# Kernel tuning notes

Measured on AMD Instinct MI355X. Metric: run time of the kernel, lower is better.

The kernel has to match this reference:

```python
import jax, jax.numpy as jnp
import numpy as np

EPS = 1e-12  # keras K.l2_normalize epsilon


def _l2_normalize(v, axis):
    return v * jax.lax.rsqrt(jnp.maximum(jnp.sum(v * v, axis=axis, keepdims=True), EPS))


def setup_inputs() -> dict:
    key = jax.random.key(0)
    k1, k2, k3, k4 = jax.random.split(key, 4)
    B, T, D, K, O = 32, 1024, 512, 64, 1024
    x = jax.random.normal(k1, (B, T, D), dtype=jnp.float32)
    weight = jax.random.normal(k2, (D, K), dtype=jnp.float32) * (1.0 / np.sqrt(D))
    bias = jnp.zeros((K,), dtype=jnp.float32)
    centers = jax.random.normal(k3, (K, D), dtype=jnp.float32)
    reduc_dim = jax.random.normal(k4, (D * K, O), dtype=jnp.float32) * 0.01
    return {"x": x, "weight": weight, "bias": bias, "centers": centers, "reduc_dim": reduc_dim}


def reference(x, weight, bias, centers, reduc_dim):
    # x: [B,T,D], weight: [D,K], bias: [K]
    # soft assignment: softmax over centers
    a = jax.nn.softmax(jnp.einsum('btd,dk->btk', x, weight) + bias, axis=-1)  # [B,T,K]
    # aggregate descriptors per center: batch_dot over time axis -> [B,K,D]
    x_agg = jnp.einsum('btk,btd->bkd', a, x)
    # total soft weight per center: [B,K]
    sum_w = jnp.sum(a, axis=1)
    # residual vs centers, broadcast: [B,K,D]
    full = x_agg - sum_w[:, :, None] * centers[None, :, :]
    # intra-normalize per center vector
    full = _l2_normalize(full, axis=-1)
    B = x.shape[0]
    full = full.reshape(B, -1)  # [B, K*D]
    full = _l2_normalize(full, axis=-1)
    return full @ reduc_dim  # [B, output_dim]
```

## Files before the change

### kernel.cpp

```cpp
#include <hip/hip_runtime.h>
#include <math.h>

#define TT 1024
#define DD 512
#define KK 64
#define OO 1024
#define EPSF 1e-12f

typedef __attribute__((ext_vector_type(8))) short bf16x8;
typedef __attribute__((ext_vector_type(4))) float f32x4;

__device__ __forceinline__ ushort f2bf(float f) {
  unsigned u = __float_as_uint(f);
  u = (u + 0x7FFFu + ((u >> 16) & 1u)) >> 16;
  return (ushort)u;
}
__device__ __forceinline__ float bf2f(ushort h) {
  return __uint_as_float(((unsigned)h) << 16);
}


__global__ __launch_bounds__(256) void nv_k0(const float* __restrict__ w,
                                             ushort* __restrict__ whT,
                                             float* __restrict__ sum_w) {
  int idx = blockIdx.x * 256 + threadIdx.x;
  if (idx < 32768) {
    int d = idx >> 6, k = idx & 63;
    whT[(size_t)k * DD + d] = f2bf(w[idx]);
  } else if (idx < 32768 + 2048) {
    sum_w[idx - 32768] = 0.f;
  }
}

__global__ __launch_bounds__(256) void nv_k1(
    const float* __restrict__ x, const ushort* __restrict__ whT,
    const float* __restrict__ bias, ushort* __restrict__ aT,
    ushort* __restrict__ xbfT, float* __restrict__ sum_w) {
  const int b = blockIdx.y, t0 = blockIdx.x * 64;
  const int tid = threadIdx.x;
  const int wave = tid >> 6, lane = tid & 63, l15 = lane & 15, q = lane >> 4;

  __shared__ ushort xs[64 * 64];
  __shared__ ushort xsT[64 * 64];
  __shared__ ushort wsm[64 * 64];

  f32x4 acc[4];
#pragma unroll
  for (int nt = 0; nt < 4; ++nt)
#pragma unroll
    for (int r = 0; r < 4; ++r) acc[nt][r] = 0.f;

  for (int dc = 0; dc < DD; dc += 64) {
    __syncthreads();
#pragma unroll
    for (int it = 0; it < 2; ++it) {
      int gi = it * 256 + tid;
      int t = gi >> 3, gd = gi & 7;
      const float* px = x + (size_t)(b * TT + t0 + t) * DD + dc + gd * 8;
      float4 v0 = *(const float4*)px;
      float4 v1 = *(const float4*)(px + 4);
      ushort u[8];
      u[0] = f2bf(v0.x); u[1] = f2bf(v0.y); u[2] = f2bf(v0.z); u[3] = f2bf(v0.w);
      u[4] = f2bf(v1.x); u[5] = f2bf(v1.y); u[6] = f2bf(v1.z); u[7] = f2bf(v1.w);
      bf16x8 pk;
#pragma unroll
      for (int i = 0; i < 8; ++i) pk[i] = (short)u[i];
      *(bf16x8*)(xs + t * 64 + ((gd ^ (t & 7)) << 3)) = pk;
      int tg = t >> 3;
#pragma unroll
      for (int i = 0; i < 8; ++i) {
        int d = gd * 8 + i;
        xsT[d * 64 + ((tg ^ ((d >> 3) & 7)) << 3) + (t & 7)] = u[i];
      }
    }
#pragma unroll
    for (int it = 0; it < 2; ++it) {
      int gi = it * 256 + tid;
      int k = gi >> 3, gd = gi & 7;
      bf16x8 v = *(const bf16x8*)(whT + (size_t)k * DD + dc + gd * 8);
      *(bf16x8*)(wsm + k * 64 + ((gd ^ (k & 7)) << 3)) = v;
    }
    __syncthreads();
#pragma unroll
    for (int kc = 0; kc < 2; ++kc) {
      int gq = kc * 4 + q;
      int t = wave * 16 + l15;
      bf16x8 af = *(const bf16x8*)(xs + t * 64 + ((gq ^ (t & 7)) << 3));
#pragma unroll
      for (int nt = 0; nt < 4; ++nt) {
        int k = nt * 16 + l15;
        bf16x8 bfv = *(const bf16x8*)(wsm + k * 64 + ((gq ^ (k & 7)) << 3));
        acc[nt] = __builtin_amdgcn_mfma_f32_16x16x32_bf16(af, bfv, acc[nt], 0, 0, 0);
      }
    }
#pragma unroll
    for (int it = 0; it < 2; ++it) {
      int gi = it * 256 + tid;
      int d = gi >> 3, g = gi & 7;
      bf16x8 v = *(const bf16x8*)(xsT + d * 64 + (g << 3));
      int tg = g ^ ((d >> 3) & 7);
      *(bf16x8*)(xbfT + (size_t)(b * DD + dc + d) * TT + t0 + tg * 8) = v;
    }
  }

  float bia[4];
#pragma unroll
  for (int nt = 0; nt < 4; ++nt) bia[nt] = bias[nt * 16 + l15];

  ushort au[4][4];
  float sw[4] = {0.f, 0.f, 0.f, 0.f};
#pragma unroll
  for (int r = 0; r < 4; ++r) {
    float l[4];
#pragma unroll
    for (int nt = 0; nt < 4; ++nt) l[nt] = acc[nt][r] + bia[nt];
    float m = fmaxf(fmaxf(l[0], l[1]), fmaxf(l[2], l[3]));
#pragma unroll
    for (int s = 1; s <= 8; s <<= 1) m = fmaxf(m, __shfl_xor(m, s));
    float e[4];
#pragma unroll
    for (int nt = 0; nt < 4; ++nt) e[nt] = __expf(l[nt] - m);
    float ssum = e[0] + e[1] + e[2] + e[3];
#pragma unroll
    for (int s = 1; s <= 8; s <<= 1) ssum += __shfl_xor(ssum, s);
    float inv = 1.f / ssum;
#pragma unroll
    for (int nt = 0; nt < 4; ++nt) {
      ushort u = f2bf(e[nt] * inv);
      au[nt][r] = u;
      sw[nt] += bf2f(u);
    }
  }
#pragma unroll
  for (int nt = 0; nt < 4; ++nt) {
    float s = sw[nt];
    s += __shfl_xor(s, 16);
    s += __shfl_xor(s, 32);
    if (q == 0) atomicAdd(sum_w + b * KK + nt * 16 + l15, s);
  }
  __syncthreads();
#pragma unroll
  for (int nt = 0; nt < 4; ++nt)
#pragma unroll
    for (int r = 0; r < 4; ++r) {
      int k = nt * 16 + l15;
      int t = wave * 16 + q * 4 + r;
      xs[k * 64 + (((t >> 3) ^ (k & 7)) << 3) + (t & 7)] = au[nt][r];
    }
  __syncthreads();
#pragma unroll
  for (int it = 0; it < 2; ++it) {
    int gi = it * 256 + tid;
    int k = gi >> 3, g = gi & 7;
    bf16x8 v = *(const bf16x8*)(xs + k * 64 + (g << 3));
    int tg = g ^ (k & 7);
    *(bf16x8*)(aT + (size_t)(b * KK + k) * TT + t0 + tg * 8) = v;
  }
}

__global__ __launch_bounds__(256) void nv_k2(
    const ushort* __restrict__ aT, const ushort* __restrict__ xbfT,
    float* __restrict__ xaggP) {
  const int d0 = blockIdx.x * 64;
  const int b = blockIdx.y;
  const int tsp = blockIdx.z;
  const int tid = threadIdx.x;
  const int wave = tid >> 6, lane = tid & 63, l15 = lane & 15, q = lane >> 4;

  __shared__ ushort asx[64 * 64];
  __shared__ ushort xsb[64 * 64];

  f32x4 acc[4];
#pragma unroll
  for (int nt = 0; nt < 4; ++nt)
#pragma unroll
    for (int r = 0; r < 4; ++r) acc[nt][r] = 0.f;

  for (int tc = 0; tc < 4; ++tc) {
    const int t0 = tsp * 256 + tc * 64;
    __syncthreads();
#pragma unroll
    for (int it = 0; it < 2; ++it) {
      int gi = it * 256 + tid;
      int k = gi >> 3, g = gi & 7;
      bf16x8 v = *(const bf16x8*)(aT + (size_t)(b * KK + k) * TT + t0 + g * 8);
      *(bf16x8*)(asx + k * 64 + ((g ^ (k & 7)) << 3)) = v;
    }
#pragma unroll
    for (int it = 0; it < 2; ++it) {
      int gi = it * 256 + tid;
      int d = gi >> 3, g = gi & 7;
      bf16x8 v = *(const bf16x8*)(xbfT + (size_t)(b * DD + d0 + d) * TT + t0 + g * 8);
      *(bf16x8*)(xsb + d * 64 + ((g ^ (d & 7)) << 3)) = v;
    }
    __syncthreads();
#pragma unroll
    for (int kc = 0; kc < 2; ++kc) {
      int gq = kc * 4 + q;
      int k = wave * 16 + l15;
      bf16x8 af = *(const bf16x8*)(asx + k * 64 + ((gq ^ (k & 7)) << 3));
#pragma unroll
      for (int nt = 0; nt < 4; ++nt) {
        int d = nt * 16 + l15;
        bf16x8 bfv = *(const bf16x8*)(xsb + d * 64 + ((gq ^ (d & 7)) << 3));
        acc[nt] = __builtin_amdgcn_mfma_f32_16x16x32_bf16(af, bfv, acc[nt], 0, 0, 0);
      }
    }
  }
#pragma unroll
  for (int nt = 0; nt < 4; ++nt)
#pragma unroll
    for (int r = 0; r < 4; ++r) {
      int k = wave * 16 + q * 4 + r;
      xaggP[(size_t)((tsp * 32 + b) * KK + k) * DD + d0 + nt * 16 + l15] = acc[nt][r];
    }
}

__global__ __launch_bounds__(128) void nv_k3a(
    const float* __restrict__ xaggP, float* __restrict__ full,
    const float* __restrict__ centers, const float* __restrict__ sum_w,
    float* __restrict__ s1) {
  const int k = blockIdx.x, b = blockIdx.y;
  const int tid = threadIdx.x;
  const float sw = sum_w[b * KK + k];
  float4 v = make_float4(0.f, 0.f, 0.f, 0.f);
#pragma unroll
  for (int sp = 0; sp < 4; ++sp) {
    float4 p = *((const float4*)(xaggP + (size_t)((sp * 32 + b) * KK + k) * DD) + tid);
    v.x += p.x; v.y += p.y; v.z += p.z; v.w += p.w;
  }
  float4 c = *((const float4*)(centers + (size_t)k * DD) + tid);
  v.x = fmaf(-sw, c.x, v.x);
  v.y = fmaf(-sw, c.y, v.y);
  v.z = fmaf(-sw, c.z, v.z);
  v.w = fmaf(-sw, c.w, v.w);
  *((float4*)(full + (size_t)(b * KK + k) * DD) + tid) = v;
  float ss = v.x * v.x + v.y * v.y + v.z * v.z + v.w * v.w;
#pragma unroll
  for (int s = 1; s <= 32; s <<= 1) ss += __shfl_xor(ss, s);
  __shared__ float red[2];
  if ((tid & 63) == 0) red[tid >> 6] = ss;
  __syncthreads();
  if (tid == 0) s1[b * KK + k] = red[0] + red[1];
}

__global__ __launch_bounds__(64) void nv_k3b(const float* __restrict__ s1,
                                             float* __restrict__ scale) {
  const int b = blockIdx.x, k = threadIdx.x;
  float r = s1[b * KK + k];
  float d1 = fmaxf(r, EPSF);
  float s2 = r / d1;
#pragma unroll
  for (int s = 1; s <= 32; s <<= 1) s2 += __shfl_xor(s2, s);
  scale[b * KK + k] = rsqrtf(d1) * rsqrtf(fmaxf(s2, EPSF));
}

__global__ __launch_bounds__(128) void nv_k3c(const float* __restrict__ full,
                                              const float* __restrict__ scale,
                                              ushort* __restrict__ fullbf) {
  const int blk = blockIdx.x;
  const float sc = scale[blk];
  float4 v = *((const float4*)(full + (size_t)blk * DD) + threadIdx.x);
  ushort4 o;
  o.x = f2bf(v.x * sc); o.y = f2bf(v.y * sc);
  o.z = f2bf(v.z * sc); o.w = f2bf(v.w * sc);
  *((ushort4*)(fullbf + (size_t)blk * DD) + threadIdx.x) = o;
}

__global__ __launch_bounds__(256) void nv_k4(
    const ushort* __restrict__ fullbf, const float* __restrict__ reduc,
    float* __restrict__ outP) {
  const int c_base = blockIdx.x * 64;
  const int r_base = blockIdx.y * 512;
  const int tid = threadIdx.x;
  const int tx = tid & 15;
  const int ty = (tid >> 4) & 3;
  const int tz = tid >> 6;
  const int c0 = c_base + tx * 4;

  __shared__ float As2[32 * 128];

  float acc[8][4] = {};

  for (int ch = 0; ch < 4; ++ch) {
    const int rch = r_base + ch * 128;
    __syncthreads();
#pragma unroll
    for (int it = 0; it < 2; ++it) {
      int gi = it * 256 + tid;
      int bb = gi >> 4, g = gi & 15;
      bf16x8 v = *(const bf16x8*)(fullbf + (size_t)bb * 32768 + rch + g * 8);
      float4 lo, hi;
      lo.x = bf2f((ushort)v[0]); lo.y = bf2f((ushort)v[1]);
      lo.z = bf2f((ushort)v[2]); lo.w = bf2f((ushort)v[3]);
      hi.x = bf2f((ushort)v[4]); hi.y = bf2f((ushort)v[5]);
      hi.z = bf2f((ushort)v[6]); hi.w = bf2f((ushort)v[7]);
      *(float4*)(As2 + bb * 128 + g * 8) = lo;
      *(float4*)(As2 + bb * 128 + g * 8 + 4) = hi;
    }
    __syncthreads();
#pragma unroll 4
    for (int i = 0; i < 8; ++i) {
      const int rl = i * 16 + ty * 4;
      float wv[4][4];
#pragma unroll
      for (int j = 0; j < 4; ++j) {
        float4 w = *(const float4*)(reduc + (size_t)(rch + rl + j) * OO + c0);
        wv[j][0] = w.x; wv[j][1] = w.y; wv[j][2] = w.z; wv[j][3] = w.w;
      }
#pragma unroll
      for (int bb = 0; bb < 8; ++bb) {
        float4 a4 = *(const float4*)(As2 + (tz * 8 + bb) * 128 + rl);
        float a_[4] = {a4.x, a4.y, a4.z, a4.w};
#pragma unroll
        for (int j = 0; j < 4; ++j) {
          acc[bb][0] = fmaf(a_[j], wv[j][0], acc[bb][0]);
          acc[bb][1] = fmaf(a_[j], wv[j][1], acc[bb][1]);
          acc[bb][2] = fmaf(a_[j], wv[j][2], acc[bb][2]);
          acc[bb][3] = fmaf(a_[j], wv[j][3], acc[bb][3]);
        }
      }
    }
  }

#pragma unroll
  for (int bb = 0; bb < 8; ++bb) {
    float4 v = make_float4(acc[bb][0], acc[bb][1], acc[bb][2], acc[bb][3]);
    v.x += __shfl_xor(v.x, 16); v.x += __shfl_xor(v.x, 32);
    v.y += __shfl_xor(v.y, 16); v.y += __shfl_xor(v.y, 32);
    v.z += __shfl_xor(v.z, 16); v.z += __shfl_xor(v.z, 32);
    v.w += __shfl_xor(v.w, 16); v.w += __shfl_xor(v.w, 32);
    if (ty == 0) {
      *(float4*)(outP + (size_t)(blockIdx.y * 32 + tz * 8 + bb) * OO + c0) = v;
    }
  }
}

__global__ __launch_bounds__(256) void nv_k5(const float* __restrict__ outP,
                                             float* __restrict__ out) {
  const int idx = blockIdx.x * 256 + threadIdx.x;
  float s = 0.f;
#pragma unroll 8
  for (int sp = 0; sp < 64; ++sp) s += outP[(size_t)sp * 32768 + idx];
  out[idx] = s;
}

extern "C" void kernel_launch(void* const* d_in, const int* in_sizes, int n_in,
                              void* d_out, int out_size, void* d_ws, size_t ws_size,
                              hipStream_t stream) {
  const float* x = (const float*)d_in[0];
  const float* weight = (const float*)d_in[1];
  const float* bias = (const float*)d_in[2];
  const float* centers = (const float*)d_in[3];
  const float* reduc = (const float*)d_in[4];
  float* out = (float*)d_out;
  float* ws = (float*)d_ws;

  ushort* aT = (ushort*)ws;
  ushort* xbfT = (ushort*)(ws + 1048576);
  float* xaggP = ws + 9437184;
  float* full = ws + 13631488;
  ushort* fullbf = (ushort*)(ws + 14680064);
  float* outP = ws + 15728640;
  ushort* whT = (ushort*)(ws + 17825792);
  float* sum_w = ws + 17825792 + 16384;
  float* s1 = sum_w + 2048;
  float* scale = sum_w + 4096;

  nv_k0<<<136, 256, 0, stream>>>(weight, whT, sum_w);
  nv_k1<<<dim3(16, 32), 256, 0, stream>>>(x, whT, bias, aT, xbfT, sum_w);
  nv_k2<<<dim3(8, 32, 4), 256, 0, stream>>>(aT, xbfT, xaggP);
  nv_k3a<<<dim3(64, 32), 128, 0, stream>>>(xaggP, full, centers, sum_w, s1);
  nv_k3b<<<32, 64, 0, stream>>>(s1, scale);
  nv_k3c<<<2048, 128, 0, stream>>>(full, scale, fullbf);
  nv_k4<<<dim3(16, 64), 256, 0, stream>>>(fullbf, reduc, outP);
  nv_k5<<<128, 256, 0, stream>>>(outP, out);
}
```

Before: 319.4 us.

## Restructure final projection GEMM with transposed fp32 activations and wider split-K

```diff
diff --git a/kernel.cpp b/kernel.cpp
--- a/kernel.cpp
+++ b/kernel.cpp
@@ -257,82 +257,93 @@
 
 __global__ __launch_bounds__(128) void nv_k3c(const float* __restrict__ full,
                                               const float* __restrict__ scale,
-                                              ushort* __restrict__ fullbf) {
+                                              float* __restrict__ fullT) {
   const int blk = blockIdx.x;
+  const int b = blk >> 6, k = blk & 63;
   const float sc = scale[blk];
   float4 v = *((const float4*)(full + (size_t)blk * DD) + threadIdx.x);
-  ushort4 o;
-  o.x = f2bf(v.x * sc); o.y = f2bf(v.y * sc);
-  o.z = f2bf(v.z * sc); o.w = f2bf(v.w * sc);
-  *((ushort4*)(fullbf + (size_t)blk * DD) + threadIdx.x) = o;
-}
-
-__global__ __launch_bounds__(256) void nv_k4(
-    const ushort* __restrict__ fullbf, const float* __restrict__ reduc,
+  int r0 = k * DD + threadIdx.x * 4;
+  fullT[(size_t)(r0 + 0) * 32 + b] = v.x * sc;
+  fullT[(size_t)(r0 + 1) * 32 + b] = v.y * sc;
+  fullT[(size_t)(r0 + 2) * 32 + b] = v.z * sc;
+  fullT[(size_t)(r0 + 3) * 32 + b] = v.w * sc;
+}
+
+__global__ __launch_bounds__(256, 2) void nv_k4(
+    const float* __restrict__ fullT, const float* __restrict__ reduc,
     float* __restrict__ outP) {
-  const int c_base = blockIdx.x * 64;
-  const int r_base = blockIdx.y * 512;
+  const int strip = blockIdx.x;
+  const int ksp = blockIdx.y;
   const int tid = threadIdx.x;
-  const int tx = tid & 15;
-  const int ty = (tid >> 4) & 3;
-  const int tz = tid >> 6;
-  const int c0 = c_base + tx * 4;
-
-  __shared__ float As2[32 * 128];
-
-  float acc[8][4] = {};
-
-  for (int ch = 0; ch < 4; ++ch) {
-    const int rch = r_base + ch * 128;
-    __syncthreads();
-#pragma unroll
-    for (int it = 0; it < 2; ++it) {
-      int gi = it * 256 + tid;
-      int bb = gi >> 4, g = gi & 15;
-      bf16x8 v = *(const bf16x8*)(fullbf + (size_t)bb * 32768 + rch + g * 8);
-      float4 lo, hi;
-      lo.x = bf2f((ushort)v[0]); lo.y = bf2f((ushort)v[1]);
-      lo.z = bf2f((ushort)v[2]); lo.w = bf2f((ushort)v[3]);
-      hi.x = bf2f((ushort)v[4]); hi.y = bf2f((ushort)v[5]);
-      hi.z = bf2f((ushort)v[6]); hi.w = bf2f((ushort)v[7]);
-      *(float4*)(As2 + bb * 128 + g * 8) = lo;
-      *(float4*)(As2 + bb * 128 + g * 8 + 4) = hi;
-    }
-    __syncthreads();
-#pragma unroll 4
-    for (int i = 0; i < 8; ++i) {
-      const int rl = i * 16 + ty * 4;
-      float wv[4][4];
-#pragma unroll
-      for (int j = 0; j < 4; ++j) {
-        float4 w = *(const float4*)(reduc + (size_t)(rch + rl + j) * OO + c0);
-        wv[j][0] = w.x; wv[j][1] = w.y; wv[j][2] = w.z; wv[j][3] = w.w;
-      }
-#pragma unroll
-      for (int bb = 0; bb < 8; ++bb) {
-        float4 a4 = *(const float4*)(As2 + (tz * 8 + bb) * 128 + rl);
-        float a_[4] = {a4.x, a4.y, a4.z, a4.w};
-#pragma unroll
-        for (int j = 0; j < 4; ++j) {
-          acc[bb][0] = fmaf(a_[j], wv[j][0], acc[bb][0]);
-          acc[bb][1] = fmaf(a_[j], wv[j][1], acc[bb][1]);
-          acc[bb][2] = fmaf(a_[j], wv[j][2], acc[bb][2]);
-          acc[bb][3] = fmaf(a_[j], wv[j][3], acc[bb][3]);
+  const int wave = tid >> 6, lane = tid & 63;
+  const int c0 = strip * 256 + lane * 4;
+  const int kblk = ksp * 256;
+
+  __shared__ float fst[256 * 32];
+
+#pragma unroll
+  for (int it = 0; it < 8; ++it) {
+    int f4 = it * 256 + tid;
+    *(float4*)(fst + f4 * 4) = *(const float4*)(fullT + (size_t)kblk * 32 + f4 * 4);
+  }
+  __syncthreads();
+
+  float4 acc[32];
+#pragma unroll
+  for (int b = 0; b < 32; ++b) acc[b] = make_float4(0.f, 0.f, 0.f, 0.f);
+
+  const int kw = wave * 64;
+#pragma unroll 2
+  for (int kk = 0; kk < 64; ++kk) {
+    const int kl = kw + kk;
+    float4 rv = *(const float4*)(reduc + (size_t)(kblk + kl) * OO + c0);
+#pragma unroll
+    for (int b4 = 0; b4 < 8; ++b4) {
+      float4 fv = *(const float4*)(fst + kl * 32 + b4 * 4);
+      acc[b4 * 4 + 0].x = fmaf(fv.x, rv.x, acc[b4 * 4 + 0].x);
+      acc[b4 * 4 + 0].y = fmaf(fv.x, rv.y, acc[b4 * 4 + 0].y);
+      acc[b4 * 4 + 0].z = fmaf(fv.x, rv.z, acc[b4 * 4 + 0].z);
+      acc[b4 * 4 + 0].w = fmaf(fv.x, rv.w, acc[b4 * 4 + 0].w);
+      acc[b4 * 4 + 1].x = fmaf(fv.y, rv.x, acc[b4 * 4 + 1].x);
+      acc[b4 * 4 + 1].y = fmaf(fv.y, rv.y, acc[b4 * 4 + 1].y);
+      acc[b4 * 4 + 1].z = fmaf(fv.y, rv.z, acc[b4 * 4 + 1].z);
+      acc[b4 * 4 + 1].w = fmaf(fv.y, rv.w, acc[b4 * 4 + 1].w);
+      acc[b4 * 4 + 2].x = fmaf(fv.z, rv.x, acc[b4 * 4 + 2].x);
+      acc[b4 * 4 + 2].y = fmaf(fv.z, rv.y, acc[b4 * 4 + 2].y);
+      acc[b4 * 4 + 2].z = fmaf(fv.z, rv.z, acc[b4 * 4 + 2].z);
+      acc[b4 * 4 + 2].w = fmaf(fv.z, rv.w, acc[b4 * 4 + 2].w);
+      acc[b4 * 4 + 3].x = fmaf(fv.w, rv.x, acc[b4 * 4 + 3].x);
+      acc[b4 * 4 + 3].y = fmaf(fv.w, rv.y, acc[b4 * 4 + 3].y);
+      acc[b4 * 4 + 3].z = fmaf(fv.w, rv.z, acc[b4 * 4 + 3].z);
+      acc[b4 * 4 + 3].w = fmaf(fv.w, rv.w, acc[b4 * 4 + 3].w);
+    }
+  }
+
+  __syncthreads();
+  for (int w = 0; w < 4; ++w) {
+    if (wave == w) {
+      if (w == 0) {
+#pragma unroll
+        for (int b = 0; b < 32; ++b)
+          *(float4*)(fst + b * 256 + lane * 4) = acc[b];
+      } else {
+#pragma unroll
+        for (int b = 0; b < 32; ++b) {
+          float4 v = *(float4*)(fst + b * 256 + lane * 4);
+          v.x += acc[b].x; v.y += acc[b].y; v.z += acc[b].z; v.w += acc[b].w;
+          *(float4*)(fst + b * 256 + lane * 4) = v;
         }
       }
     }
-  }
-
-#pragma unroll
-  for (int bb = 0; bb < 8; ++bb) {
-    float4 v = make_float4(acc[bb][0], acc[bb][1], acc[bb][2], acc[bb][3]);
-    v.x += __shfl_xor(v.x, 16); v.x += __shfl_xor(v.x, 32);
-    v.y += __shfl_xor(v.y, 16); v.y += __shfl_xor(v.y, 32);
-    v.z += __shfl_xor(v.z, 16); v.z += __shfl_xor(v.z, 32);
-    v.w += __shfl_xor(v.w, 16); v.w += __shfl_xor(v.w, 32);
-    if (ty == 0) {
-      *(float4*)(outP + (size_t)(blockIdx.y * 32 + tz * 8 + bb) * OO + c0) = v;
-    }
+    __syncthreads();
+  }
+
+#pragma unroll
+  for (int it = 0; it < 8; ++it) {
+    int f4 = it * 256 + tid;
+    int b = f4 >> 6, cg = f4 & 63;
+    *(float4*)(outP + ((size_t)(ksp * 32 + b) * OO) + strip * 256 + cg * 4) =
+        *(const float4*)(fst + b * 256 + cg * 4);
   }
 }
 
@@ -341,7 +352,7 @@
   const int idx = blockIdx.x * 256 + threadIdx.x;
   float s = 0.f;
 #pragma unroll 8
-  for (int sp = 0; sp < 64; ++sp) s += outP[(size_t)sp * 32768 + idx];
+  for (int sp = 0; sp < 128; ++sp) s += outP[(size_t)sp * 32768 + idx];
   out[idx] = s;
 }
 
@@ -360,10 +371,10 @@
   ushort* xbfT = (ushort*)(ws + 1048576);
   float* xaggP = ws + 9437184;
   float* full = ws + 13631488;
-  ushort* fullbf = (ushort*)(ws + 14680064);
+  float* fullT = ws + 14680064;
   float* outP = ws + 15728640;
-  ushort* whT = (ushort*)(ws + 17825792);
-  float* sum_w = ws + 17825792 + 16384;
+  ushort* whT = (ushort*)(ws + 19922944);
+  float* sum_w = ws + 19922944 + 16384;
   float* s1 = sum_w + 2048;
   float* scale = sum_w + 4096;
 
@@ -372,7 +383,7 @@
   nv_k2<<<dim3(8, 32, 4), 256, 0, stream>>>(aT, xbfT, xaggP);
   nv_k3a<<<dim3(64, 32), 128, 0, stream>>>(xaggP, full, centers, sum_w, s1);
   nv_k3b<<<32, 64, 0, stream>>>(s1, scale);
-  nv_k3c<<<2048, 128, 0, stream>>>(full, scale, fullbf);
-  nv_k4<<<dim3(16, 64), 256, 0, stream>>>(fullbf, reduc, outP);
+  nv_k3c<<<2048, 128, 0, stream>>>(full, scale, fullT);
+  nv_k4<<<dim3(4, 128), 256, 0, stream>>>(fullT, reduc, outP);
   nv_k5<<<128, 256, 0, stream>>>(outP, out);
 }
```

After: 293.3 us. 1.09x faster.
